# Kernel tuning notes

Measured on AMD Instinct MI355X. Metric: run time of the kernel, lower is better.

## Reference

```python
import jax, jax.numpy as jnp
import numpy as np

N, T, H, NENV, L = 8192, 48, 256, 10, 2
NIN = 1 + 2 + NENV + 1 + 2  # x, coords(2), env(NENV), areas, bird_uv(2) = 16


def setup_inputs() -> dict:
    key = jax.random.key(0)
    ks = jax.random.split(key, 10)
    x = jax.random.normal(ks[0], (N, T), dtype=jnp.float32)
    coords = jax.random.normal(ks[1], (N, 2), dtype=jnp.float32)
    env = jax.random.normal(ks[2], (N, NENV, T), dtype=jnp.float32)
    areas = jax.random.uniform(ks[3], (N,), dtype=jnp.float32)
    bird_uv = jax.random.normal(ks[4], (N, 2, T), dtype=jnp.float32)
    # input2hidden: Linear(NIN, H, bias=False), kaiming-normal (fan_in = NIN)
    W_in = jax.random.normal(ks[5], (H, NIN), dtype=jnp.float32) * np.sqrt(2.0 / NIN)
    # LSTMCell params per layer: weight_ih [4H,H], weight_hh [4H,H], biases [4H]
    k_lstm = 1.0 / np.sqrt(H)
    W_ih = jax.random.uniform(ks[6], (L, 4 * H, H), minval=-k_lstm, maxval=k_lstm, dtype=jnp.float32)
    W_hh = jax.random.uniform(ks[7], (L, 4 * H, H), minval=-k_lstm, maxval=k_lstm, dtype=jnp.float32)
    b_ih = jax.random.uniform(ks[8], (L, 4 * H), minval=-k_lstm, maxval=k_lstm, dtype=jnp.float32)
    b_hh = jax.random.uniform(ks[9], (L, 4 * H), minval=-k_lstm, maxval=k_lstm, dtype=jnp.float32)
    return {"x": x, "coords": coords, "env": env, "areas": areas, "bird_uv": bird_uv,
            "W_in": W_in, "W_ih": W_ih, "W_hh": W_hh, "b_ih": b_ih, "b_hh": b_hh}


def _lstm_cell(inp, h, c, w_ih, w_hh, bi, bh):
    # torch.nn.LSTMCell gate order: i, f, g, o
    gates = inp @ w_ih.T + bi + h @ w_hh.T + bh  # [N, 4H]
    i, f, g, o = jnp.split(gates, 4, axis=-1)
    i = jax.nn.sigmoid(i)
    f = jax.nn.sigmoid(f)
    g = jnp.tanh(g)
    o = jax.nn.sigmoid(o)
    c_new = f * c + i * g
    h_new = o * jnp.tanh(c_new)
    return h_new, c_new


def reference(x, coords, env, areas, bird_uv, W_in, W_ih, W_hh, b_ih, b_hh):
    # Build [N, NIN, T] feature tensor matching torch.cat([x, coords, env, areas, bird_uv], dim=1)
    feats = jnp.concatenate([
        x[:, None, :],                                            # [N,1,T]
        jnp.broadcast_to(coords[:, :, None], (N, 2, T)),          # [N,2,T]
        env,                                                      # [N,NENV,T]
        jnp.broadcast_to(areas[:, None, None], (N, 1, T)),        # [N,1,T]
        bird_uv,                                                  # [N,2,T]
    ], axis=1)
    # input2hidden applied to all timesteps at once: [T, N, H]
    proj = jnp.einsum('hf,nft->tnh', W_in, feats)

    def step(carry, inp_t):
        h, c = carry  # each [L, N, H]
        inp = inp_t
        hs, cs = [], []
        for l in range(L):  # dropout_p = 0 -> no dropout between layers
            hl, cl = _lstm_cell(inp, h[l], c[l], W_ih[l], W_hh[l], b_ih[l], b_hh[l])
            hs.append(hl)
            cs.append(cl)
            inp = hl
        return (jnp.stack(hs), jnp.stack(cs)), None

    h0 = jnp.zeros((L, N, H), dtype=x.dtype)
    c0 = jnp.zeros((L, N, H), dtype=x.dtype)
    (h, c), _ = jax.lax.scan(step, (h0, c0), proj)
    return h, c
```

## Files before the change

### kernel.cpp

```cpp
#include <hip/hip_runtime.h>
#include <hip/hip_bf16.h>
#include <cstdint>

#define NB 8192
#define TSTEPS 48

typedef __hip_bfloat16 bf16;
typedef short bf16x8 __attribute__((ext_vector_type(8)));
typedef float f32x4 __attribute__((ext_vector_type(4)));

__device__ __forceinline__ float sigf(float x) { return 1.0f / (1.0f + __expf(-x)); }
__device__ __forceinline__ float tanhf_fast(float x) { return 2.0f / (1.0f + __expf(-2.0f * x)) - 1.0f; }

__device__ __forceinline__ void gld_lds16(const void* g, void* l) {
  typedef const __attribute__((address_space(1))) unsigned int* gp_t;
  typedef __attribute__((address_space(3))) unsigned int* lp_t;
  __builtin_amdgcn_global_load_lds(reinterpret_cast<gp_t>(reinterpret_cast<uintptr_t>(g)),
                                   reinterpret_cast<lp_t>(reinterpret_cast<uintptr_t>(l)),
                                   16, 0, 0);
}

__device__ __forceinline__ int orig_row_p(int p) {
  int ug = p >> 6, g = (p >> 4) & 3, s = p & 15;
  return g * 256 + ug * 16 + s;
}
__device__ __forceinline__ int unswz_col(int colp, int r) {
  int cc = ((colp >> 3) & 3) ^ ((r >> 1) & 3);
  return (colp & ~31) | (cc << 3) | (colp & 7);
}

__global__ void feats_kernel(const float* __restrict__ x, const float* __restrict__ coords,
                             const float* __restrict__ env, const float* __restrict__ areas,
                             const float* __restrict__ bird, bf16* __restrict__ feats) {
  int idx = blockIdx.x * 256 + threadIdx.x;
  int n = idx & (NB - 1);
  int t = idx >> 13;
  __align__(16) bf16 v[32];
  v[0] = __float2bfloat16(x[n * TSTEPS + t]);
  v[1] = __float2bfloat16(coords[n * 2 + 0]);
  v[2] = __float2bfloat16(coords[n * 2 + 1]);
#pragma unroll
  for (int e = 0; e < 10; ++e) v[3 + e] = __float2bfloat16(env[(n * 10 + e) * TSTEPS + t]);
  v[13] = __float2bfloat16(areas[n]);
  v[14] = __float2bfloat16(bird[(n * 2 + 0) * TSTEPS + t]);
  v[15] = __float2bfloat16(bird[(n * 2 + 1) * TSTEPS + t]);
#pragma unroll
  for (int f = 16; f < 32; ++f) v[f] = __float2bfloat16(0.0f);
  bf16* dst = feats + (size_t)idx * 32;
  int sw = (n >> 1) & 3;
#pragma unroll
  for (int c = 0; c < 4; ++c) ((bf16x8*)dst)[c ^ sw] = ((const bf16x8*)v)[c];
}

__global__ void packA_kernel(const float* __restrict__ W_hh0, const float* __restrict__ W_ih0,
                             const float* __restrict__ W_in, bf16* __restrict__ WA) {
  int idx = blockIdx.x * 256 + threadIdx.x;
  int p = idx / 288, colp = idx % 288;
  int j = orig_row_p(p);
  int k = unswz_col(colp, p);
  float val = 0.0f;
  if (k < 256) {
    val = W_hh0[j * 256 + k];
  } else if (k < 272) {
    int f = k - 256;
    float s = 0.0f;
    for (int kk = 0; kk < 256; ++kk) s += W_ih0[j * 256 + kk] * W_in[kk * 16 + f];
    val = s;
  }
  WA[(size_t)p * 288 + colp] = __float2bfloat16(val);
}

__global__ void packB_kernel(const float* __restrict__ W_ih1, const float* __restrict__ W_hh1,
                             bf16* __restrict__ WB) {
  int idx = blockIdx.x * 256 + threadIdx.x;
  int p = idx >> 9, colp = idx & 511;
  int j = orig_row_p(p);
  int k = unswz_col(colp, p);
  float val = (k < 256) ? W_ih1[j * 256 + k] : W_hh1[j * 256 + (k - 256)];
  WB[(size_t)p * 512 + colp] = __float2bfloat16(val);
}

__global__ void packBias_kernel(const float* __restrict__ b_ih, const float* __restrict__ b_hh,
                                float* __restrict__ bA, float* __restrict__ bB) {
  int idx = blockIdx.x * 256 + threadIdx.x;
  int layer = idx >> 10, r = idx & 1023;
  float v = b_ih[layer * 1024 + r] + b_hh[layer * 1024 + r];
  if (layer == 0) bA[r] = v; else bB[r] = v;
}

__global__ __launch_bounds__(256, 4) void lstm_step(
    const bf16* __restrict__ h0r, bf16* __restrict__ h0w,
    const bf16* __restrict__ h1r, bf16* __restrict__ h1w,
    const bf16* __restrict__ feats,
    const bf16* __restrict__ WA, const bf16* __restrict__ WB,
    const float* __restrict__ bA, const float* __restrict__ bB,
    bf16* __restrict__ c0, bf16* __restrict__ c1,
    float* __restrict__ out, int tA, int tB, int phase0, int lastA, int lastB) {
  __shared__ __align__(16) bf16 As[2 * 128 * 32];
  __shared__ __align__(16) bf16 Bs[2 * 128 * 32];

  const int tid = threadIdx.x;
  const int wid = tid >> 6, lane = tid & 63;
  const int quad = lane >> 4, l16 = lane & 15;
  const int mb = (wid >> 1) * 64, nb = (wid & 1) * 64;
  const int rowbase = blockIdx.x * 128;
  const int q = blockIdx.y;
  const int isA = blockIdx.z + phase0;

  const bf16* Wp = isA ? WA : WB;
  const int KW = isA ? 288 : 512;
  const int KITERS = isA ? 9 : 16;

  f32x4 acc[4][4];
#pragma unroll
  for (int i = 0; i < 4; ++i)
#pragma unroll
    for (int j = 0; j < 4; ++j) acc[i][j] = f32x4{0.f, 0.f, 0.f, 0.f};

  const int r4 = lane >> 2;
  const int ch = (lane & 3) * 8;
  const int cb = (quad ^ ((l16 >> 1) & 3)) * 8;
  const int arow = wid * 32 + r4;
  const bf16* WGrow = Wp + (size_t)(q * 128 + arow) * KW + ch;

  auto stage = [&](int kb, int buf) {
    const bf16* asrc;
    int astr;
    if (isA && kb == 8) {
      asrc = feats + (size_t)tA * (NB * 32);
      astr = 32;
    } else if (!isA && kb >= 8) {
      asrc = h1r + (kb - 8) * 32;
      astr = 256;
    } else {
      asrc = h0r + kb * 32;
      astr = 256;
    }
    const bf16* ga = asrc + (size_t)(rowbase + arow) * astr + ch;
    bf16* lA = As + buf * (128 * 32) + wid * (32 * 32);
    gld_lds16(ga, lA);
    gld_lds16(ga + (size_t)16 * astr, lA + 16 * 32);
    const bf16* gb = WGrow + kb * 32;
    bf16* lB = Bs + buf * (128 * 32) + wid * (32 * 32);
    gld_lds16(gb, lB);
    gld_lds16(gb + (size_t)16 * KW, lB + 16 * 32);
  };

  stage(0, 0);
  __syncthreads();

  for (int kb = 0; kb < KITERS; ++kb) {
    const int buf = kb & 1;
    if (kb + 1 < KITERS) stage(kb + 1, buf ^ 1);
    const bf16* Ab = As + buf * (128 * 32);
    const bf16* Bb = Bs + buf * (128 * 32);
    bf16x8 af[4], bfr[4];
#pragma unroll
    for (int i = 0; i < 4; ++i) af[i] = *(const bf16x8*)(Ab + (mb + i * 16 + l16) * 32 + cb);
#pragma unroll
    for (int j = 0; j < 4; ++j) bfr[j] = *(const bf16x8*)(Bb + (nb + j * 16 + l16) * 32 + cb);
#pragma unroll
    for (int i = 0; i < 4; ++i)
#pragma unroll
      for (int j = 0; j < 4; ++j)
        acc[i][j] = __builtin_amdgcn_mfma_f32_16x16x32_bf16(af[i], bfr[j], acc[i][j], 0, 0, 0);
    if (kb + 1 < KITERS) __syncthreads();
  }

  const int u = (q * 2 + (nb >> 6)) * 16 + l16;
  const float* bias = isA ? bA : bB;
  bf16* cst = isA ? c0 : c1;
  bf16* hout = isA ? h0w : h1w;
  const int last = isA ? lastA : lastB;
  float* out_h = out + (size_t)(isA ? 0 : 1) * NB * 256;
  float* out_c = out + (size_t)(isA ? 2 : 3) * NB * 256;
  const float bi = bias[u], bf_ = bias[256 + u], bg = bias[512 + u], bo = bias[768 + u];
#pragma unroll
  for (int i = 0; i < 4; ++i) {
#pragma unroll
    for (int rr = 0; rr < 4; ++rr) {
      const int n = rowbase + mb + i * 16 + quad * 4 + rr;
      const size_t ci = (size_t)n * 256 + u;
      float gi = sigf(acc[i][0][rr] + bi);
      float gf = sigf(acc[i][1][rr] + bf_);
      float gg = tanhf_fast(acc[i][2][rr] + bg);
      float go = sigf(acc[i][3][rr] + bo);
      float c = __bfloat162float(cst[ci]);
      float cn = gf * c + gi * gg;
      float hn = go * tanhf_fast(cn);
      if (!last) cst[ci] = __float2bfloat16(cn);
      const int col = (u & ~31) | ((((u >> 3) & 3) ^ ((n >> 1) & 3)) << 3) | (u & 7);
      hout[(size_t)n * 256 + col] = __float2bfloat16(hn);
      if (last) { out_h[ci] = hn; out_c[ci] = cn; }
    }
  }
}

extern "C" void kernel_launch(void* const* d_in, const int* in_sizes, int n_in,
                              void* d_out, int out_size, void* d_ws, size_t ws_size,
                              hipStream_t stream) {
  const float* x = (const float*)d_in[0];
  const float* coords = (const float*)d_in[1];
  const float* env = (const float*)d_in[2];
  const float* areas = (const float*)d_in[3];
  const float* bird = (const float*)d_in[4];
  const float* W_in = (const float*)d_in[5];
  const float* W_ih = (const float*)d_in[6];
  const float* W_hh = (const float*)d_in[7];
  const float* b_ih = (const float*)d_in[8];
  const float* b_hh = (const float*)d_in[9];
  float* out = (float*)d_out;

  const size_t MB = 1 << 20;
  char* w0 = (char*)d_ws;
  auto H0 = [&](int i) { return (bf16*)(w0 + (size_t)i * 8 * MB); };
  auto H1 = [&](int i) { return (bf16*)(w0 + 4 * MB + (size_t)i * 8 * MB); };
  bf16* c0 = (bf16*)(w0 + 16 * MB);
  bf16* c1 = (bf16*)(w0 + 20 * MB);
  bf16* feats = (bf16*)(w0 + 24 * MB);
  bf16* WA = (bf16*)(w0 + 48 * MB);
  bf16* WB = (bf16*)(w0 + 49 * MB);
  float* bA = (float*)(w0 + 50 * MB);
  float* bB = (float*)(w0 + 50 * MB + 4096);

  hipMemsetAsync(w0 + 8 * MB, 0, 16 * MB, stream);

  feats_kernel<<<(NB * TSTEPS) / 256, 256, 0, stream>>>(x, coords, env, areas, bird, feats);
  packA_kernel<<<(1024 * 288) / 256, 256, 0, stream>>>(W_hh, W_ih, W_in, WA);
  packB_kernel<<<(1024 * 512) / 256, 256, 0, stream>>>(W_ih + 1024 * 256, W_hh + 1024 * 256, WB);
  packBias_kernel<<<2048 / 256, 256, 0, stream>>>(b_ih, b_hh, bA, bB);

  lstm_step<<<dim3(64, 8, 1), 256, 0, stream>>>(
      H0(1), H0(0), H1(0), H1(1), feats, WA, WB, bA, bB, c0, c1, out,
      0, 0, 1, 0, 0);
  for (int s2 = 0; s2 <= 46; ++s2) {
    int pa = (s2 + 1) & 1, pb = s2 & 1;
    lstm_step<<<dim3(64, 8, 2), 256, 0, stream>>>(
        H0(pb), H0(pa), H1(pa), H1(pb), feats, WA, WB, bA, bB, c0, c1, out,
        s2 + 1, s2, 0, (s2 == 46), 0);
  }
  lstm_step<<<dim3(64, 8, 1), 256, 0, stream>>>(
      H0(1), H0(0), H1(0), H1(1), feats, WA, WB, bA, bB, c0, c1, out,
      0, 47, 0, 0, 1);
}
```

Measured before the change: 1.376 ms.

## Triple-buffer activation tiles with explicit vmcnt waits and MFMA priority

Splits the LDS staging into separate activation and weight loaders, gives the activation tile three LDS buffers so it is prefetched two k-steps ahead, and replaces __syncthreads with explicit s_waitcnt vmcnt counts plus raw barriers. The MFMA block is also wrapped in s_setprio. The aim is to hide global-to-LDS latency behind compute in this short K loop. The cost is extra LDS per block, which may reduce occupancy at 4 blocks per CU, and the hand-counted vmcnt values can break if the compiler emits other memory operations.

```diff
diff --git a/kernel.cpp b/kernel.cpp
--- a/kernel.cpp
+++ b/kernel.cpp
@@ -96,7 +96,7 @@
     const float* __restrict__ bA, const float* __restrict__ bB,
     bf16* __restrict__ c0, bf16* __restrict__ c1,
     float* __restrict__ out, int tA, int tB, int phase0, int lastA, int lastB) {
-  __shared__ __align__(16) bf16 As[2 * 128 * 32];
+  __shared__ __align__(16) bf16 As[3 * 128 * 32];
   __shared__ __align__(16) bf16 Bs[2 * 128 * 32];
 
   const int tid = threadIdx.x;
@@ -123,7 +123,7 @@
   const int arow = wid * 32 + r4;
   const bf16* WGrow = Wp + (size_t)(q * 128 + arow) * KW + ch;
 
-  auto stage = [&](int kb, int buf) {
+  auto stageA = [&](int kb, int buf) {
     const bf16* asrc;
     int astr;
     if (isA && kb == 8) {
@@ -140,31 +140,52 @@
     bf16* lA = As + buf * (128 * 32) + wid * (32 * 32);
     gld_lds16(ga, lA);
     gld_lds16(ga + (size_t)16 * astr, lA + 16 * 32);
+  };
+  auto stageB = [&](int kb, int buf) {
     const bf16* gb = WGrow + kb * 32;
     bf16* lB = Bs + buf * (128 * 32) + wid * (32 * 32);
     gld_lds16(gb, lB);
     gld_lds16(gb + (size_t)16 * KW, lB + 16 * 32);
   };
 
-  stage(0, 0);
-  __syncthreads();
-
+  stageB(0, 0);
+  stageA(0, 0);
+  stageA(1, 1);
+
+  int abuf = 0;
   for (int kb = 0; kb < KITERS; ++kb) {
-    const int buf = kb & 1;
-    if (kb + 1 < KITERS) stage(kb + 1, buf ^ 1);
-    const bf16* Ab = As + buf * (128 * 32);
-    const bf16* Bb = Bs + buf * (128 * 32);
+    if (kb + 1 < KITERS) stageB(kb + 1, (kb + 1) & 1);
+    if (kb + 2 < KITERS) {
+      int a2 = abuf + 2;
+      stageA(kb + 2, a2 >= 3 ? a2 - 3 : a2);
+      asm volatile("s_waitcnt vmcnt(6)" ::: "memory");
+    } else if (kb + 1 < KITERS) {
+      asm volatile("s_waitcnt vmcnt(4)" ::: "memory");
+    } else {
+      asm volatile("s_waitcnt vmcnt(0)" ::: "memory");
+    }
+    __builtin_amdgcn_s_barrier();
+
+    const bf16* Ab = As + abuf * (128 * 32);
+    const bf16* Bb = Bs + (kb & 1) * (128 * 32);
     bf16x8 af[4], bfr[4];
 #pragma unroll
     for (int i = 0; i < 4; ++i) af[i] = *(const bf16x8*)(Ab + (mb + i * 16 + l16) * 32 + cb);
 #pragma unroll
     for (int j = 0; j < 4; ++j) bfr[j] = *(const bf16x8*)(Bb + (nb + j * 16 + l16) * 32 + cb);
+    __builtin_amdgcn_s_setprio(1);
 #pragma unroll
     for (int i = 0; i < 4; ++i)
 #pragma unroll
       for (int j = 0; j < 4; ++j)
         acc[i][j] = __builtin_amdgcn_mfma_f32_16x16x32_bf16(af[i], bfr[j], acc[i][j], 0, 0, 0);
-    if (kb + 1 < KITERS) __syncthreads();
+    __builtin_amdgcn_s_setprio(0);
+
+    if (kb + 1 < KITERS) {
+      asm volatile("s_waitcnt lgkmcnt(0)" ::: "memory");
+      __builtin_amdgcn_s_barrier();
+    }
+    abuf = (abuf + 1 == 3) ? 0 : abuf + 1;
   }
 
   const int u = (q * 2 + (nb >> 6)) * 16 + l16;
```

Result: slower. 1.446 ms (+5.1%).
